# Kernel optimization log

Measured on AMD Instinct MI355X. Metric: run time of the kernel, lower is better.

## Reference

```python
import jax, jax.numpy as jnp
import numpy as np
import math

H = 4            # cross_attn_heads
SPARSE_RATIO = 0.6
B, N, C = 128, 196, 768


def setup_inputs() -> dict:
    key = jax.random.key(0)
    ks = jax.random.split(key, 10)
    xav = (6.0 / (C + C)) ** 0.5  # xavier_uniform bound for square Linear
    inp = {
        "RGB_cash": jax.random.normal(ks[0], (B, N, C), jnp.float32),
        "NI_cash": jax.random.normal(ks[1], (B, N, C), jnp.float32),
        "TI_cash": jax.random.normal(ks[2], (B, N, C), jnp.float32),
        "RGB_global": jax.random.normal(ks[3], (B, C), jnp.float32),
        "NI_global": jax.random.normal(ks[4], (B, C), jnp.float32),
        "TI_global": jax.random.normal(ks[5], (B, C), jnp.float32),
        # 9 CrossModalAttention modules, stacked: q_proj / k_proj weights (out,in) and biases
        "q_w": jax.random.uniform(ks[6], (9, C, C), jnp.float32, -xav, xav),
        "q_b": jnp.zeros((9, C), jnp.float32),
        "k_w": jax.random.uniform(ks[7], (9, C, C), jnp.float32, -xav, xav),
        "k_b": jnp.zeros((9, C), jnp.float32),
        # 3 TokenSparse modal_weights, init torch.ones(3); small noise for non-degenerate softmax
        "modal_w": jnp.ones((3, 3), jnp.float32) + 0.01 * jax.random.normal(ks[8], (3, 3), jnp.float32),
    }
    return inp


def _cos_sim(patches, g):
    # patches (B,N,C), g (B,C) -> (B,N); F.normalize eps=1e-12
    pn = patches / jnp.maximum(jnp.linalg.norm(patches, axis=-1, keepdims=True), 1e-12)
    gn = g / jnp.maximum(jnp.linalg.norm(g, axis=-1, keepdims=True), 1e-12)
    return jnp.einsum("bnc,bc->bn", pn, gn)


def _cross_attn(patches, g, cos, qw, qb, kw, kb):
    # CrossModalAttention.forward: Q from global (1 token), K from patches, softmax over N
    b, n, c = patches.shape
    d = c // H
    q = (g @ qw.T + qb).reshape(b, H, d)              # (B,H,D)
    k = (patches @ kw.T + kb).reshape(b, n, H, d)     # (B,N,H,D)
    attn = jnp.einsum("bhd,bnhd->bhn", q, k) * (d ** -0.5)
    attn = jax.nn.softmax(attn, axis=-1)              # (B,H,N)
    return (attn * cos[:, None, :]).mean(axis=1)      # (B,N)


def _minmax(s):
    smin = s.min(axis=-1, keepdims=True)
    smax = s.max(axis=-1, keepdims=True)
    return (s - smin) / (smax - smin + 1e-8)


def _token_sparse(tokens, s_im, s_m2, s_m3, mw):
    b, n, c = tokens.shape
    w = jax.nn.softmax(mw)
    score = w[0] * _minmax(s_im) + w[1] * _minmax(s_m2) + w[2] * _minmax(s_m3)
    num_keep = max(1, math.ceil(n * SPARSE_RATIO))
    _, idx = jax.lax.top_k(score, num_keep)           # == descending sort, first num_keep
    mask = jnp.zeros((b, n), score.dtype).at[jnp.arange(b)[:, None], idx].set(1.0)
    return tokens * mask[..., None], mask


def reference(RGB_cash, NI_cash, TI_cash, RGB_global, NI_global, TI_global,
              q_w, q_b, k_w, k_b, modal_w):
    toks = [RGB_cash, NI_cash, TI_cash]
    glbs = [RGB_global, NI_global, TI_global]
    # module order: rgb_self, rgb_x_nir, rgb_x_tir, nir_self, nir_x_rgb, nir_x_tir,
    #               tir_self, tir_x_rgb, tir_x_nir
    order = [(0, 0), (0, 1), (0, 2), (1, 1), (1, 0), (1, 2), (2, 2), (2, 0), (2, 1)]
    scores = []
    for i, (pi, gi) in enumerate(order):
        cos = _cos_sim(toks[pi], glbs[gi])
        scores.append(_cross_attn(toks[pi], glbs[gi], cos, q_w[i], q_b[i], k_w[i], k_b[i]))
    out_rgb, m_rgb = _token_sparse(RGB_cash, scores[0], scores[1], scores[2], modal_w[0])
    out_nir, m_nir = _token_sparse(NI_cash, scores[3], scores[4], scores[5], modal_w[1])
    out_tir, m_tir = _token_sparse(TI_cash, scores[6], scores[7], scores[8], modal_w[2])
    return (out_rgb, out_nir, out_tir, m_rgb, m_nir, m_tir)
```

## Files before the change

### kernel.cpp

```cpp
#include <hip/hip_runtime.h>
#include <math.h>

#define BB   128
#define NN   196
#define CC   768
#define HH   4
#define DD   192
#define TOK_PER   19267584
#define NROWS_ALL 75264
#define F4_ALL    14450688
#define NUM_KEEP  118
#define SCALE_D   0.07216878364870322f

#define OFF_QPART 0
#define SZ_QPART  (2*9*128*768)
#define OFF_VV    (OFF_QPART + SZ_QPART)
#define SZ_VV     (9*128*4*768)
#define OFF_BIAS  (OFF_VV + SZ_VV)
#define SZ_BIAS   (9*128*4)
#define OFF_GN    (OFF_BIAS + SZ_BIAS)
#define SZ_GN     (3*128*768)
#define OFF_SC    (OFF_GN + SZ_GN)
#define SZ_SC     (3*128*196*16)

__device__ __forceinline__ float4 f4fma(float s, float4 b, float4 a) {
  a.x = fmaf(s, b.x, a.x); a.y = fmaf(s, b.y, a.y);
  a.z = fmaf(s, b.z, a.z); a.w = fmaf(s, b.w, a.w);
  return a;
}
__device__ __forceinline__ float f4dot(float4 p, float4 q) {
  return p.x*q.x + p.y*q.y + p.z*q.z + p.w*q.w;
}

__global__ __launch_bounds__(256) void k_qproj(const float* __restrict__ g0,
                                               const float* __restrict__ g1,
                                               const float* __restrict__ g2,
                                               const float* __restrict__ qw,
                                               float* __restrict__ qpart) {
  __shared__ __align__(16) float AsT[32 * 68];
  __shared__ __align__(16) float WsT[32 * 68];
  const int gtab[9] = {0, 1, 2, 1, 0, 2, 2, 0, 1};
  int i = blockIdx.y, z = blockIdx.z;
  int mt = blockIdx.x & 1, nt = blockIdx.x >> 1;
  int tid = threadIdx.x, tx = tid & 15, ty = tid >> 4;
  int gi = gtab[i];
  const float4* A4 = (const float4*)((gi == 0) ? g0 : ((gi == 1) ? g1 : g2));
  const float4* W4 = (const float4*)(qw + (size_t)i * CC * CC);
  float4 acc0 = {0,0,0,0}, acc1 = {0,0,0,0}, acc2 = {0,0,0,0}, acc3 = {0,0,0,0};
  int arow = mt * 64, wrow = nt * 64;
  int kb4 = z * 96;
  for (int kk = 0; kk < 12; kk++) {
    #pragma unroll
    for (int f = tid; f < 512; f += 256) {
      int r = f >> 3, k4 = f & 7;
      float4 va = A4[(size_t)(arow + r) * 192 + kb4 + kk * 8 + k4];
      float4 vw = W4[(size_t)(wrow + r) * 192 + kb4 + kk * 8 + k4];
      int kq = 4 * k4;
      AsT[(kq+0)*68 + r] = va.x; AsT[(kq+1)*68 + r] = va.y;
      AsT[(kq+2)*68 + r] = va.z; AsT[(kq+3)*68 + r] = va.w;
      WsT[(kq+0)*68 + r] = vw.x; WsT[(kq+1)*68 + r] = vw.y;
      WsT[(kq+2)*68 + r] = vw.z; WsT[(kq+3)*68 + r] = vw.w;
    }
    __syncthreads();
    #pragma unroll
    for (int k = 0; k < 32; k++) {
      float4 a = *(const float4*)&AsT[k * 68 + 4 * ty];
      float4 w = *(const float4*)&WsT[k * 68 + 4 * tx];
      acc0 = f4fma(a.x, w, acc0); acc1 = f4fma(a.y, w, acc1);
      acc2 = f4fma(a.z, w, acc2); acc3 = f4fma(a.w, w, acc3);
    }
    __syncthreads();
  }
  float* dst = qpart + (size_t)(z * 9 + i) * 128 * CC;
  int col = wrow + 4 * tx;
  int row = arow + 4 * ty;
  *(float4*)&dst[(size_t)(row + 0) * CC + col] = acc0;
  *(float4*)&dst[(size_t)(row + 1) * CC + col] = acc1;
  *(float4*)&dst[(size_t)(row + 2) * CC + col] = acc2;
  *(float4*)&dst[(size_t)(row + 3) * CC + col] = acc3;
}

__global__ __launch_bounds__(256) void k_vvproj(const float* __restrict__ qpart,
                                                const float* __restrict__ qb,
                                                const float* __restrict__ kw,
                                                float* __restrict__ vvout) {
  __shared__ __align__(16) float AsT[32 * 68];
  __shared__ __align__(16) float Bs[32 * 68];
  int ih = blockIdx.y; int i = ih >> 2, h = ih & 3;
  int mt = blockIdx.x & 1, nt = blockIdx.x >> 1;
  int tid = threadIdx.x, tx = tid & 15, ty = tid >> 4;
  const float4* qp0 = (const float4*)qpart + (size_t)i * 128 * 192;
  const float4* qp1 = (const float4*)qpart + (size_t)(9 + i) * 128 * 192;
  const float4* qb4 = (const float4*)qb + (size_t)i * 192;
  const float4* B4  = (const float4*)(kw + (size_t)i * CC * CC);
  float4 acc0 = {0,0,0,0}, acc1 = {0,0,0,0}, acc2 = {0,0,0,0}, acc3 = {0,0,0,0};
  int arow = mt * 64;
  int bcol4 = nt * 16;
  for (int kk = 0; kk < 6; kk++) {
    #pragma unroll
    for (int f = tid; f < 512; f += 256) {
      int r = f >> 3, k4 = f & 7;
      int colf4 = h * 48 + kk * 8 + k4;
      float4 va = qp0[(size_t)(arow + r) * 192 + colf4];
      float4 vb = qp1[(size_t)(arow + r) * 192 + colf4];
      float4 vq = qb4[colf4];
      va.x += vb.x + vq.x; va.y += vb.y + vq.y;
      va.z += vb.z + vq.z; va.w += vb.w + vq.w;
      int kq = 4 * k4;
      AsT[(kq+0)*68 + r] = va.x; AsT[(kq+1)*68 + r] = va.y;
      AsT[(kq+2)*68 + r] = va.z; AsT[(kq+3)*68 + r] = va.w;
      int rk = f >> 4, c4 = f & 15;
      float4 vB = B4[(size_t)(h * DD + kk * 32 + rk) * 192 + bcol4 + c4];
      *(float4*)&Bs[rk * 68 + 4 * c4] = vB;
    }
    __syncthreads();
    #pragma unroll
    for (int k = 0; k < 32; k++) {
      float4 a = *(const float4*)&AsT[k * 68 + 4 * ty];
      float4 bb = *(const float4*)&Bs[k * 68 + 4 * tx];
      acc0 = f4fma(a.x, bb, acc0); acc1 = f4fma(a.y, bb, acc1);
      acc2 = f4fma(a.z, bb, acc2); acc3 = f4fma(a.w, bb, acc3);
    }
    __syncthreads();
  }
  int col = nt * 64 + 4 * tx;
  int b0 = arow + 4 * ty;
  *(float4*)&vvout[((size_t)(i * 128 + b0 + 0) * 4 + h) * CC + col] = acc0;
  *(float4*)&vvout[((size_t)(i * 128 + b0 + 1) * 4 + h) * CC + col] = acc1;
  *(float4*)&vvout[((size_t)(i * 128 + b0 + 2) * 4 + h) * CC + col] = acc2;
  *(float4*)&vvout[((size_t)(i * 128 + b0 + 3) * 4 + h) * CC + col] = acc3;
}

__global__ __launch_bounds__(256) void k_bias(const float* __restrict__ qpart,
                                              const float* __restrict__ qb,
                                              const float* __restrict__ kb,
                                              float* __restrict__ bias) {
  int ih = blockIdx.x; int i = ih >> 2, h = ih & 3;
  int w = threadIdx.x >> 6, lane = threadIdx.x & 63;
  const float* qbb = qb + (size_t)i * CC + h * DD;
  const float* kbb = kb + (size_t)i * CC + h * DD;
  float kb0 = kbb[lane], kb1 = kbb[lane + 64], kb2 = kbb[lane + 128];
  float qb0 = qbb[lane], qb1 = qbb[lane + 64], qb2 = qbb[lane + 128];
  const float* q0base = qpart + (size_t)i * 128 * CC + h * DD;
  const float* q1base = qpart + (size_t)(9 + i) * 128 * CC + h * DD;
  for (int b = w; b < 128; b += 4) {
    const float* q0 = q0base + (size_t)b * CC;
    const float* q1 = q1base + (size_t)b * CC;
    float s = (q0[lane]       + q1[lane]       + qb0) * kb0
            + (q0[lane + 64]  + q1[lane + 64]  + qb1) * kb1
            + (q0[lane + 128] + q1[lane + 128] + qb2) * kb2;
    #pragma unroll
    for (int off = 32; off; off >>= 1) s += __shfl_xor(s, off);
    if (lane == 0) bias[((size_t)i * 128 + b) * 4 + h] = s;
  }
}

__global__ __launch_bounds__(256, 2) void k_dots2(const float* __restrict__ rgb,
                                                  const float* __restrict__ ni,
                                                  const float* __restrict__ ti,
                                                  const float* __restrict__ vv,
                                                  const float* __restrict__ g0,
                                                  const float* __restrict__ g1,
                                                  const float* __restrict__ g2,
                                                  const float* __restrict__ bias,
                                                  float* __restrict__ sc) {
  __shared__ float red[4][64 * 17];
  __shared__ __align__(16) float GN[3 * CC];
  int bid = blockIdx.x;
  int t = bid >> 8;
  int rem = bid & 255;
  int b = rem >> 1, half = rem & 1;
  int tid = threadIdx.x;
  int w = tid >> 6, lane = tid & 63;
  const float* toks = (t == 0) ? rgb : ((t == 1) ? ni : ti);
  int gi0, gi1, gi2;
  if (t == 0)      { gi0 = 0; gi1 = 1; gi2 = 2; }
  else if (t == 1) { gi0 = 1; gi1 = 0; gi2 = 2; }
  else             { gi0 = 2; gi1 = 0; gi2 = 1; }

  if (w < 3) {
    int gidx = (w == 0) ? gi0 : ((w == 1) ? gi1 : gi2);
    const float* gsrc = (gidx == 0) ? g0 : ((gidx == 1) ? g1 : g2);
    const float4* s4 = (const float4*)(gsrc + (size_t)b * CC);
    float4 u0 = s4[lane], u1 = s4[lane + 64], u2 = s4[lane + 128];
    float ss = f4dot(u0, u0) + f4dot(u1, u1) + f4dot(u2, u2);
    #pragma unroll
    for (int off = 32; off; off >>= 1) ss += __shfl_xor(ss, off);
    float inv = 1.0f / fmaxf(sqrtf(ss), 1e-12f);
    u0.x *= inv; u0.y *= inv; u0.z *= inv; u0.w *= inv;
    u1.x *= inv; u1.y *= inv; u1.z *= inv; u1.w *= inv;
    u2.x *= inv; u2.y *= inv; u2.z *= inv; u2.w *= inv;
    float4* d4 = (float4*)&GN[w * CC];
    d4[lane] = u0; d4[lane + 64] = u1; d4[lane + 128] = u2;
  }

  float4 V[36];
  #pragma unroll
  for (int k = 0; k < 3; k++) {
    #pragma unroll
    for (int h = 0; h < 4; h++) {
      const float4* src = (const float4*)(vv + (((size_t)(3*t + k) * 128 + b) * 4 + h) * CC);
      int v = k * 4 + h;
      V[3*v + 0] = src[lane];
      V[3*v + 1] = src[lane + 64];
      V[3*v + 2] = src[lane + 128];
    }
  }

  int a_id = lane & 15;
  float bias_r = 0.f;
  if (a_id < 12)
    bias_r = bias[((size_t)(3*t + (a_id >> 2)) * 128 + b) * 4 + (a_id & 3)];

  __syncthreads();

  float* myred = red[w];
  const float4* G4 = (const float4*)GN;
  int s_grp = lane >> 4;
  int n0 = half * 98;

  const float4* pr0 = (const float4*)(toks + ((size_t)b * NN + n0 + w) * CC);
  float4 pc0 = pr0[lane], pc1 = pr0[lane + 64], pc2 = pr0[lane + 128];

  for (int it = 0; it < 25; it++) {
    int row_local = it * 4 + w;
    if (row_local >= 98) break;

    int rl_next = row_local + 4;
    float4 pn0 = pc0, pn1 = pc1, pn2 = pc2;
    if (rl_next < 98) {
      const float4* pr = (const float4*)(toks + ((size_t)b * NN + n0 + rl_next) * CC);
      pn0 = pr[lane]; pn1 = pr[lane + 64]; pn2 = pr[lane + 128];
    }

    float a[16];
    #pragma unroll
    for (int v = 0; v < 12; v++)
      a[v] = f4dot(pc0, V[3*v]) + f4dot(pc1, V[3*v + 1]) + f4dot(pc2, V[3*v + 2]);
    #pragma unroll
    for (int j = 0; j < 3; j++)
      a[12 + j] = f4dot(pc0, G4[j*192 + lane])
                + f4dot(pc1, G4[j*192 + lane + 64])
                + f4dot(pc2, G4[j*192 + lane + 128]);
    a[15] = f4dot(pc0, pc0) + f4dot(pc1, pc1) + f4dot(pc2, pc2);

    #pragma unroll
    for (int v = 0; v < 16; v++) myred[lane * 17 + v] = a[v];
    __builtin_amdgcn_s_waitcnt(0xc07f);
    __builtin_amdgcn_sched_barrier(0);
    float part = 0.f;
    #pragma unroll
    for (int i2 = 0; i2 < 16; i2++)
      part += myred[(s_grp * 16 + i2) * 17 + a_id];
    part += __shfl_xor(part, 16, 64);
    part += __shfl_xor(part, 32, 64);

    float s15  = __shfl(part, 15, 64);
    float invp = 1.0f / fmaxf(sqrtf(s15), 1e-12f);
    float res;
    if (a_id < 12)      res = (part + bias_r) * SCALE_D;
    else if (a_id < 15) res = part * invp;
    else                res = invp;

    if (lane < 16) {
      float* scrow = sc + (((size_t)t * 128 + b) * 196 + (n0 + row_local)) * 16;
      scrow[lane] = res;
    }
    pc0 = pn0; pc1 = pn1; pc2 = pn2;
  }
}

__global__ __launch_bounds__(256) void k_score(const float* __restrict__ sc,
                                               const float* __restrict__ modal_w,
                                               float* __restrict__ outmask) {
  __shared__ float S[196 * 17];
  __shared__ float CSUM[12];
  __shared__ float SV[3][196];
  __shared__ float MN[3], MX[3];
  __shared__ float sfinal[196];
  int b = blockIdx.x, m = blockIdx.y;
  int tid = threadIdx.x;
  int w = tid >> 6, lane = tid & 63;
  bool act = tid < NN;

  const float4* base = (const float4*)(sc + ((size_t)m * 128 + b) * 196 * 16);
  if (act) {
    float4 r0 = base[tid*4+0], r1 = base[tid*4+1], r2 = base[tid*4+2], r3 = base[tid*4+3];
    float* d = &S[tid * 17];
    d[0] = r0.x; d[1] = r0.y; d[2]  = r0.z; d[3]  = r0.w;
    d[4] = r1.x; d[5] = r1.y; d[6]  = r1.z; d[7]  = r1.w;
    d[8] = r2.x; d[9] = r2.y; d[10] = r2.z; d[11] = r2.w;
    d[12] = r3.x; d[13] = r3.y; d[14] = r3.z;
  }
  __syncthreads();

  #pragma unroll
  for (int c = w; c < 12; c += 4) {
    int n3 = lane + 192;
    float v0 = S[(lane      ) * 17 + c];
    float v1 = S[(lane +  64) * 17 + c];
    float v2 = S[(lane + 128) * 17 + c];
    float v3 = (n3 < NN) ? S[n3 * 17 + c] : -3.4e38f;
    float mx = fmaxf(fmaxf(v0, v1), fmaxf(v2, v3));
    #pragma unroll
    for (int off = 32; off; off >>= 1) mx = fmaxf(mx, __shfl_xor(mx, off));
    float e0 = expf(v0 - mx), e1 = expf(v1 - mx), e2 = expf(v2 - mx);
    float e3 = (n3 < NN) ? expf(v3 - mx) : 0.f;
    float es = e0 + e1 + e2 + e3;
    #pragma unroll
    for (int off = 32; off; off >>= 1) es += __shfl_xor(es, off);
    S[(lane      ) * 17 + c] = e0;
    S[(lane +  64) * 17 + c] = e1;
    S[(lane + 128) * 17 + c] = e2;
    if (n3 < NN) S[n3 * 17 + c] = e3;
    if (lane == 0) CSUM[c] = es;
  }
  __syncthreads();

  float scv0 = 0.f, scv1 = 0.f, scv2 = 0.f;
  if (act) {
    const float* r = &S[tid * 17];
    float as0 = r[0]/CSUM[0] + r[1]/CSUM[1] + r[2]/CSUM[2]  + r[3]/CSUM[3];
    float as1 = r[4]/CSUM[4] + r[5]/CSUM[5] + r[6]/CSUM[6]  + r[7]/CSUM[7];
    float as2 = r[8]/CSUM[8] + r[9]/CSUM[9] + r[10]/CSUM[10] + r[11]/CSUM[11];
    scv0 = r[12] * as0 * 0.25f;
    scv1 = r[13] * as1 * 0.25f;
    scv2 = r[14] * as2 * 0.25f;
    SV[0][tid] = scv0; SV[1][tid] = scv1; SV[2][tid] = scv2;
  }
  __syncthreads();

  if (w < 3) {
    float u0 = SV[w][lane], u1 = SV[w][lane + 64], u2 = SV[w][lane + 128];
    float mn = fminf(fminf(u0, u1), u2);
    float mx = fmaxf(fmaxf(u0, u1), u2);
    if (lane + 192 < NN) {
      float u3 = SV[w][lane + 192];
      mn = fminf(mn, u3); mx = fmaxf(mx, u3);
    }
    #pragma unroll
    for (int off = 32; off; off >>= 1) {
      mn = fminf(mn, __shfl_xor(mn, off));
      mx = fmaxf(mx, __shfl_xor(mx, off));
    }
    if (lane == 0) { MN[w] = mn; MX[w] = mx; }
  }
  __syncthreads();

  float w0 = modal_w[m * 3 + 0], w1 = modal_w[m * 3 + 1], w2 = modal_w[m * 3 + 2];
  float wm = fmaxf(w0, fmaxf(w1, w2));
  float ew0 = expf(w0 - wm), ew1 = expf(w1 - wm), ew2 = expf(w2 - wm);
  float esum = ew0 + ew1 + ew2;
  float fv = 0.f;
  if (act) {
    fv = (ew0 / esum) * (scv0 - MN[0]) / (MX[0] - MN[0] + 1e-8f)
       + (ew1 / esum) * (scv1 - MN[1]) / (MX[1] - MN[1] + 1e-8f)
       + (ew2 / esum) * (scv2 - MN[2]) / (MX[2] - MN[2] + 1e-8f);
    sfinal[tid] = fv;
  }
  __syncthreads();

  if (act) {
    int cnt = 0;
    for (int j = 0; j < NN; j++) {
      float fj = sfinal[j];
      cnt += (fj > fv) || (fj == fv && j < tid);
    }
    outmask[((size_t)m * 128 + b) * NN + tid] = (cnt < NUM_KEEP) ? 1.0f : 0.0f;
  }
}

__global__ __launch_bounds__(256) void k_write(const float* __restrict__ rgb,
                                               const float* __restrict__ ni,
                                               const float* __restrict__ ti,
                                               const float* __restrict__ maskbuf,
                                               float* __restrict__ out) {
  int idx = blockIdx.x * 256 + threadIdx.x;
  int r = idx / 192;
  int c4 = idx - r * 192;
  int m = r / 25088;
  int rb = r - m * 25088;
  float mv = maskbuf[r];
  const float* src = (m == 0) ? rgb : ((m == 1) ? ni : ti);
  float4 o = {0.f, 0.f, 0.f, 0.f};
  if (mv != 0.0f) o = ((const float4*)src)[(size_t)rb * 192 + c4];
  ((float4*)out)[idx] = o;
}

extern "C" void kernel_launch(void* const* d_in, const int* in_sizes, int n_in,
                              void* d_out, int out_size, void* d_ws, size_t ws_size,
                              hipStream_t stream) {
  const float* rgb = (const float*)d_in[0];
  const float* ni  = (const float*)d_in[1];
  const float* ti  = (const float*)d_in[2];
  const float* g0  = (const float*)d_in[3];
  const float* g1  = (const float*)d_in[4];
  const float* g2  = (const float*)d_in[5];
  const float* qw  = (const float*)d_in[6];
  const float* qb  = (const float*)d_in[7];
  const float* kw  = (const float*)d_in[8];
  const float* kb  = (const float*)d_in[9];
  const float* mw  = (const float*)d_in[10];

  float* ws    = (float*)d_ws;
  float* qpart = ws + OFF_QPART;
  float* vv    = ws + OFF_VV;
  float* bias  = ws + OFF_BIAS;
  float* sc    = ws + OFF_SC;
  float* outf  = (float*)d_out;
  float* maskb = outf + (size_t)3 * TOK_PER;

  k_qproj<<<dim3(24, 9, 2), 256, 0, stream>>>(g0, g1, g2, qw, qpart);
  k_vvproj<<<dim3(24, 36), 256, 0, stream>>>(qpart, qb, kw, vv);
  k_bias<<<36, 256, 0, stream>>>(qpart, qb, kb, bias);
  k_dots2<<<768, 256, 0, stream>>>(rgb, ni, ti, vv, g0, g1, g2, bias, sc);
  k_score<<<dim3(128, 3), 256, 0, stream>>>(sc, mw, maskb);
  k_write<<<F4_ALL / 256, 256, 0, stream>>>(rgb, ni, ti, maskb, outf);
}
```

Baseline: 556.0 us.

## Fuse bias, dot-product, scoring and masked write into one per-batch kernel

```diff
diff --git a/kernel.cpp b/kernel.cpp
--- a/kernel.cpp
+++ b/kernel.cpp
@@ -8,7 +8,6 @@
 #define DD   192
 #define TOK_PER   19267584
 #define NROWS_ALL 75264
-#define F4_ALL    14450688
 #define NUM_KEEP  118
 #define SCALE_D   0.07216878364870322f
 
@@ -16,12 +15,6 @@
 #define SZ_QPART  (2*9*128*768)
 #define OFF_VV    (OFF_QPART + SZ_QPART)
 #define SZ_VV     (9*128*4*768)
-#define OFF_BIAS  (OFF_VV + SZ_VV)
-#define SZ_BIAS   (9*128*4)
-#define OFF_GN    (OFF_BIAS + SZ_BIAS)
-#define SZ_GN     (3*128*768)
-#define OFF_SC    (OFF_GN + SZ_GN)
-#define SZ_SC     (3*128*196*16)
 
 __device__ __forceinline__ float4 f4fma(float s, float4 b, float4 a) {
   a.x = fmaf(s, b.x, a.x); a.y = fmaf(s, b.y, a.y);
@@ -131,45 +124,32 @@
   *(float4*)&vvout[((size_t)(i * 128 + b0 + 3) * 4 + h) * CC + col] = acc3;
 }
 
-__global__ __launch_bounds__(256) void k_bias(const float* __restrict__ qpart,
-                                              const float* __restrict__ qb,
-                                              const float* __restrict__ kb,
-                                              float* __restrict__ bias) {
-  int ih = blockIdx.x; int i = ih >> 2, h = ih & 3;
-  int w = threadIdx.x >> 6, lane = threadIdx.x & 63;
-  const float* qbb = qb + (size_t)i * CC + h * DD;
-  const float* kbb = kb + (size_t)i * CC + h * DD;
-  float kb0 = kbb[lane], kb1 = kbb[lane + 64], kb2 = kbb[lane + 128];
-  float qb0 = qbb[lane], qb1 = qbb[lane + 64], qb2 = qbb[lane + 128];
-  const float* q0base = qpart + (size_t)i * 128 * CC + h * DD;
-  const float* q1base = qpart + (size_t)(9 + i) * 128 * CC + h * DD;
-  for (int b = w; b < 128; b += 4) {
-    const float* q0 = q0base + (size_t)b * CC;
-    const float* q1 = q1base + (size_t)b * CC;
-    float s = (q0[lane]       + q1[lane]       + qb0) * kb0
-            + (q0[lane + 64]  + q1[lane + 64]  + qb1) * kb1
-            + (q0[lane + 128] + q1[lane + 128] + qb2) * kb2;
-    #pragma unroll
-    for (int off = 32; off; off >>= 1) s += __shfl_xor(s, off);
-    if (lane == 0) bias[((size_t)i * 128 + b) * 4 + h] = s;
-  }
-}
-
-__global__ __launch_bounds__(256, 2) void k_dots2(const float* __restrict__ rgb,
+__global__ __launch_bounds__(256, 2) void k_fused(const float* __restrict__ rgb,
                                                   const float* __restrict__ ni,
                                                   const float* __restrict__ ti,
                                                   const float* __restrict__ vv,
                                                   const float* __restrict__ g0,
                                                   const float* __restrict__ g1,
                                                   const float* __restrict__ g2,
-                                                  const float* __restrict__ bias,
-                                                  float* __restrict__ sc) {
+                                                  const float* __restrict__ qpart,
+                                                  const float* __restrict__ qb,
+                                                  const float* __restrict__ kb,
+                                                  const float* __restrict__ modal_w,
+                                                  float* __restrict__ out,
+                                                  float* __restrict__ outmask) {
   __shared__ float red[4][64 * 17];
   __shared__ __align__(16) float GN[3 * CC];
+  __shared__ float SC[196 * 17];
+  __shared__ float BIASs[12];
+  __shared__ float CSUM[12];
+  __shared__ float SV[3][196];
+  __shared__ float MN[3], MX[3];
+  __shared__ float sfinal[196];
+  __shared__ float keepf[196];
+
   int bid = blockIdx.x;
-  int t = bid >> 8;
-  int rem = bid & 255;
-  int b = rem >> 1, half = rem & 1;
+  int t = bid >> 7;
+  int b = bid & 127;
   int tid = threadIdx.x;
   int w = tid >> 6, lane = tid & 63;
   const float* toks = (t == 0) ? rgb : ((t == 1) ? ni : ti);
@@ -178,6 +158,19 @@
   else if (t == 1) { gi0 = 1; gi1 = 0; gi2 = 2; }
   else             { gi0 = 2; gi1 = 0; gi2 = 1; }
 
+  float4 V[36];
+  #pragma unroll
+  for (int k = 0; k < 3; k++) {
+    #pragma unroll
+    for (int h = 0; h < 4; h++) {
+      const float4* src = (const float4*)(vv + (((size_t)(3*t + k) * 128 + b) * 4 + h) * CC);
+      int v = k * 4 + h;
+      V[3*v + 0] = src[lane];
+      V[3*v + 1] = src[lane + 64];
+      V[3*v + 2] = src[lane + 128];
+    }
+  }
+
   if (w < 3) {
     int gidx = (w == 0) ? gi0 : ((w == 1) ? gi1 : gi2);
     const float* gsrc = (gidx == 0) ? g0 : ((gidx == 1) ? g1 : g2);
@@ -192,44 +185,42 @@
     u2.x *= inv; u2.y *= inv; u2.z *= inv; u2.w *= inv;
     float4* d4 = (float4*)&GN[w * CC];
     d4[lane] = u0; d4[lane + 64] = u1; d4[lane + 128] = u2;
-  }
-
-  float4 V[36];
-  #pragma unroll
-  for (int k = 0; k < 3; k++) {
+
+    int i = 3 * t + w;
+    const float* qbb = qb + (size_t)i * CC;
+    const float* kbb = kb + (size_t)i * CC;
+    const float* q0p = qpart + ((size_t)i * 128 + b) * CC;
+    const float* q1p = qpart + ((size_t)(9 + i) * 128 + b) * CC;
     #pragma unroll
     for (int h = 0; h < 4; h++) {
-      const float4* src = (const float4*)(vv + (((size_t)(3*t + k) * 128 + b) * 4 + h) * CC);
-      int v = k * 4 + h;
-      V[3*v + 0] = src[lane];
-      V[3*v + 1] = src[lane + 64];
-      V[3*v + 2] = src[lane + 128];
-    }
-  }
+      int j0 = h * DD + lane;
+      float s = (q0p[j0]       + q1p[j0]       + qbb[j0])       * kbb[j0]
+              + (q0p[j0 + 64]  + q1p[j0 + 64]  + qbb[j0 + 64])  * kbb[j0 + 64]
+              + (q0p[j0 + 128] + q1p[j0 + 128] + qbb[j0 + 128]) * kbb[j0 + 128];
+      #pragma unroll
+      for (int off = 32; off; off >>= 1) s += __shfl_xor(s, off);
+      if (lane == 0) BIASs[w * 4 + h] = s;
+    }
+  }
+  __syncthreads();
 
   int a_id = lane & 15;
-  float bias_r = 0.f;
-  if (a_id < 12)
-    bias_r = bias[((size_t)(3*t + (a_id >> 2)) * 128 + b) * 4 + (a_id & 3)];
-
-  __syncthreads();
+  float bias_r = (a_id < 12) ? BIASs[a_id] : 0.f;
 
   float* myred = red[w];
   const float4* G4 = (const float4*)GN;
   int s_grp = lane >> 4;
-  int n0 = half * 98;
-
-  const float4* pr0 = (const float4*)(toks + ((size_t)b * NN + n0 + w) * CC);
+
+  const float4* pr0 = (const float4*)(toks + ((size_t)b * NN + w) * CC);
   float4 pc0 = pr0[lane], pc1 = pr0[lane + 64], pc2 = pr0[lane + 128];
 
-  for (int it = 0; it < 25; it++) {
-    int row_local = it * 4 + w;
-    if (row_local >= 98) break;
-
-    int rl_next = row_local + 4;
+  for (int it = 0; it < 49; it++) {
+    int row = it * 4 + w;
+
+    int rn = row + 4;
     float4 pn0 = pc0, pn1 = pc1, pn2 = pc2;
-    if (rl_next < 98) {
-      const float4* pr = (const float4*)(toks + ((size_t)b * NN + n0 + rl_next) * CC);
+    if (rn < NN) {
+      const float4* pr = (const float4*)(toks + ((size_t)b * NN + rn) * CC);
       pn0 = pr[lane]; pn1 = pr[lane + 64]; pn2 = pr[lane + 128];
     }
 
@@ -262,45 +253,18 @@
     else if (a_id < 15) res = part * invp;
     else                res = invp;
 
-    if (lane < 16) {
-      float* scrow = sc + (((size_t)t * 128 + b) * 196 + (n0 + row_local)) * 16;
-      scrow[lane] = res;
-    }
+    if (lane < 16) SC[row * 17 + lane] = res;
     pc0 = pn0; pc1 = pn1; pc2 = pn2;
   }
-}
-
-__global__ __launch_bounds__(256) void k_score(const float* __restrict__ sc,
-                                               const float* __restrict__ modal_w,
-                                               float* __restrict__ outmask) {
-  __shared__ float S[196 * 17];
-  __shared__ float CSUM[12];
-  __shared__ float SV[3][196];
-  __shared__ float MN[3], MX[3];
-  __shared__ float sfinal[196];
-  int b = blockIdx.x, m = blockIdx.y;
-  int tid = threadIdx.x;
-  int w = tid >> 6, lane = tid & 63;
+  __syncthreads();
+
   bool act = tid < NN;
-
-  const float4* base = (const float4*)(sc + ((size_t)m * 128 + b) * 196 * 16);
-  if (act) {
-    float4 r0 = base[tid*4+0], r1 = base[tid*4+1], r2 = base[tid*4+2], r3 = base[tid*4+3];
-    float* d = &S[tid * 17];
-    d[0] = r0.x; d[1] = r0.y; d[2]  = r0.z; d[3]  = r0.w;
-    d[4] = r1.x; d[5] = r1.y; d[6]  = r1.z; d[7]  = r1.w;
-    d[8] = r2.x; d[9] = r2.y; d[10] = r2.z; d[11] = r2.w;
-    d[12] = r3.x; d[13] = r3.y; d[14] = r3.z;
-  }
-  __syncthreads();
-
-  #pragma unroll
   for (int c = w; c < 12; c += 4) {
     int n3 = lane + 192;
-    float v0 = S[(lane      ) * 17 + c];
-    float v1 = S[(lane +  64) * 17 + c];
-    float v2 = S[(lane + 128) * 17 + c];
-    float v3 = (n3 < NN) ? S[n3 * 17 + c] : -3.4e38f;
+    float v0 = SC[(lane      ) * 17 + c];
+    float v1 = SC[(lane +  64) * 17 + c];
+    float v2 = SC[(lane + 128) * 17 + c];
+    float v3 = (n3 < NN) ? SC[n3 * 17 + c] : -3.4e38f;
     float mx = fmaxf(fmaxf(v0, v1), fmaxf(v2, v3));
     #pragma unroll
     for (int off = 32; off; off >>= 1) mx = fmaxf(mx, __shfl_xor(mx, off));
@@ -309,17 +273,17 @@
     float es = e0 + e1 + e2 + e3;
     #pragma unroll
     for (int off = 32; off; off >>= 1) es += __shfl_xor(es, off);
-    S[(lane      ) * 17 + c] = e0;
-    S[(lane +  64) * 17 + c] = e1;
-    S[(lane + 128) * 17 + c] = e2;
-    if (n3 < NN) S[n3 * 17 + c] = e3;
+    SC[(lane      ) * 17 + c] = e0;
+    SC[(lane +  64) * 17 + c] = e1;
+    SC[(lane + 128) * 17 + c] = e2;
+    if (n3 < NN) SC[n3 * 17 + c] = e3;
     if (lane == 0) CSUM[c] = es;
   }
   __syncthreads();
 
   float scv0 = 0.f, scv1 = 0.f, scv2 = 0.f;
   if (act) {
-    const float* r = &S[tid * 17];
+    const float* r = &SC[tid * 17];
     float as0 = r[0]/CSUM[0] + r[1]/CSUM[1] + r[2]/CSUM[2]  + r[3]/CSUM[3];
     float as1 = r[4]/CSUM[4] + r[5]/CSUM[5] + r[6]/CSUM[6]  + r[7]/CSUM[7];
     float as2 = r[8]/CSUM[8] + r[9]/CSUM[9] + r[10]/CSUM[10] + r[11]/CSUM[11];
@@ -347,7 +311,7 @@
   }
   __syncthreads();
 
-  float w0 = modal_w[m * 3 + 0], w1 = modal_w[m * 3 + 1], w2 = modal_w[m * 3 + 2];
+  float w0 = modal_w[t * 3 + 0], w1 = modal_w[t * 3 + 1], w2 = modal_w[t * 3 + 2];
   float wm = fmaxf(w0, fmaxf(w1, w2));
   float ew0 = expf(w0 - wm), ew1 = expf(w1 - wm), ew2 = expf(w2 - wm);
   float esum = ew0 + ew1 + ew2;
@@ -366,25 +330,22 @@
       float fj = sfinal[j];
       cnt += (fj > fv) || (fj == fv && j < tid);
     }
-    outmask[((size_t)m * 128 + b) * NN + tid] = (cnt < NUM_KEEP) ? 1.0f : 0.0f;
-  }
-}
-
-__global__ __launch_bounds__(256) void k_write(const float* __restrict__ rgb,
-                                               const float* __restrict__ ni,
-                                               const float* __restrict__ ti,
-                                               const float* __restrict__ maskbuf,
-                                               float* __restrict__ out) {
-  int idx = blockIdx.x * 256 + threadIdx.x;
-  int r = idx / 192;
-  int c4 = idx - r * 192;
-  int m = r / 25088;
-  int rb = r - m * 25088;
-  float mv = maskbuf[r];
-  const float* src = (m == 0) ? rgb : ((m == 1) ? ni : ti);
-  float4 o = {0.f, 0.f, 0.f, 0.f};
-  if (mv != 0.0f) o = ((const float4*)src)[(size_t)rb * 192 + c4];
-  ((float4*)out)[idx] = o;
+    float kf = (cnt < NUM_KEEP) ? 1.0f : 0.0f;
+    keepf[tid] = kf;
+    outmask[((size_t)t * 128 + b) * NN + tid] = kf;
+  }
+  __syncthreads();
+
+  float* obase = out + ((size_t)t * 128 + b) * NN * CC;
+  for (int r = w; r < NN; r += 4) {
+    float4 o0 = {0,0,0,0}, o1 = {0,0,0,0}, o2 = {0,0,0,0};
+    if (keepf[r] != 0.0f) {
+      const float4* srcr = (const float4*)(toks + ((size_t)b * NN + r) * CC);
+      o0 = srcr[lane]; o1 = srcr[lane + 64]; o2 = srcr[lane + 128];
+    }
+    float4* dstr = (float4*)(obase + (size_t)r * CC);
+    dstr[lane] = o0; dstr[lane + 64] = o1; dstr[lane + 128] = o2;
+  }
 }
 
 extern "C" void kernel_launch(void* const* d_in, const int* in_sizes, int n_in,
@@ -405,15 +366,11 @@
   float* ws    = (float*)d_ws;
   float* qpart = ws + OFF_QPART;
   float* vv    = ws + OFF_VV;
-  float* bias  = ws + OFF_BIAS;
-  float* sc    = ws + OFF_SC;
   float* outf  = (float*)d_out;
   float* maskb = outf + (size_t)3 * TOK_PER;
 
   k_qproj<<<dim3(24, 9, 2), 256, 0, stream>>>(g0, g1, g2, qw, qpart);
   k_vvproj<<<dim3(24, 36), 256, 0, stream>>>(qpart, qb, kw, vv);
-  k_bias<<<36, 256, 0, stream>>>(qpart, qb, kb, bias);
-  k_dots2<<<768, 256, 0, stream>>>(rgb, ni, ti, vv, g0, g1, g2, bias, sc);
-  k_score<<<dim3(128, 3), 256, 0, stream>>>(sc, mw, maskb);
-  k_write<<<F4_ALL / 256, 256, 0, stream>>>(rgb, ni, ti, maskb, outf);
-}
+  k_fused<<<384, 256, 0, stream>>>(rgb, ni, ti, vv, g0, g1, g2,
+                                   qpart, qb, kb, mw, outf, maskb);
+}
```

New measurement: 525.9 us. 1.06x faster.
